# Optimization experiments

Measured on AMD Instinct MI355X. Metric: run time of the kernel, lower is better.

Reference implementation:

```python
import jax, jax.numpy as jnp
import numpy as np
import math

B, S, H, K = 512, 200, 256, 16

def setup_inputs() -> dict:
    key = jax.random.key(0)
    ks = jax.random.split(key, 8)
    scale = 1.0 / math.sqrt(H)
    return {
        "input_tensor": jax.random.normal(ks[0], (B, S, H), dtype=jnp.float32),
        "item_mask": jax.random.randint(ks[1], (B, S, 1), 0, 2) > 0,
        "time_f_w_matrix": jax.random.uniform(ks[2], (B, S, 1), dtype=jnp.float32),
        "W1": jax.random.normal(ks[3], (H, H), dtype=jnp.float32) * scale,
        "b1": jnp.zeros((H,), dtype=jnp.float32),
        "W2": jax.random.normal(ks[4], (H, H), dtype=jnp.float32) * scale,
        "b2": jnp.zeros((H,), dtype=jnp.float32),
        "W3": jax.random.normal(ks[5], (H, K), dtype=jnp.float32) * scale,
    }

def reference(input_tensor, item_mask, time_f_w_matrix, W1, b1, W2, b2, W3):
    # small MLP: two Linear+ReLU then bias-free Linear to k_interests
    h = jax.nn.relu(jnp.einsum('bsh,hd->bsd', input_tensor, W1) + b1)
    h = jax.nn.relu(jnp.einsum('bsh,hd->bsd', h, W2) + b2)
    D = jnp.einsum('bsh,hk->bsk', h, W3)              # [B,S,K]
    D = jax.nn.softmax(D, axis=-1)                    # softmax over interests
    mask = item_mask[:, :, 0:1]                       # [B,S,1] bool, broadcast over K
    D = jnp.where(mask, D, jnp.float32(-10000.0))
    D = D / jnp.float32(math.sqrt(K))
    D = jax.nn.softmax(D, axis=-2)                    # softmax over sequence
    D = time_f_w_matrix[:, :, 0:1] * D                # time weighting
    # einsum 'nij,nik->nkj': pool items into K interest vectors
    return jnp.einsum('bsh,bsk->bkh', input_tensor, D)
```

## Files before the change

### kernel.cpp

```cpp
#include <hip/hip_runtime.h>
#include <math.h>

#define HDIM 256
#define KDIM 16
#define SDIM 200
#define BDIM 512
#define NROWS (BDIM * SDIM)
#define TM 64

typedef __bf16 bf16x8 __attribute__((ext_vector_type(8)));
typedef __bf16 bf16x4 __attribute__((ext_vector_type(4)));
typedef float  f32x4  __attribute__((ext_vector_type(4)));

__global__ __launch_bounds__(256) void pack_all(
    const float* __restrict__ W1, const float* __restrict__ W2,
    const float* __restrict__ W3,
    __bf16* __restrict__ w1h, __bf16* __restrict__ w1l,
    __bf16* __restrict__ w2h, __bf16* __restrict__ w2l,
    __bf16* __restrict__ w3h, __bf16* __restrict__ w3l)
{
    int gid = blockIdx.x * 256 + threadIdx.x;
    const float* src;
    __bf16 *oh, *ol;
    int e, N;
    if (gid < 65536)       { src = W1; oh = w1h; ol = w1l; e = gid;          N = 256; }
    else if (gid < 131072) { src = W2; oh = w2h; ol = w2l; e = gid - 65536;  N = 256; }
    else if (gid < 135168) { src = W3; oh = w3h; ol = w3l; e = gid - 131072; N = 16;  }
    else return;

    int j  = e & 7;
    int n  = (e >> 3) & (N - 1);
    int kg = e >> 3; kg = (N == 256) ? (kg >> 8) : (kg >> 4);
    int k  = kg * 8 + j;
    float v = src[k * N + n];
    __bf16 h = (__bf16)v;
    oh[e] = h;
    ol[e] = (__bf16)(v - (float)h);
}

__global__ __launch_bounds__(256) void mlp_softk_mfma(
    const float* __restrict__ X, const int* __restrict__ mask,
    const __bf16* __restrict__ W1h, const __bf16* __restrict__ W1l,
    const float* __restrict__ b1,
    const __bf16* __restrict__ W2h, const __bf16* __restrict__ W2l,
    const float* __restrict__ b2,
    const __bf16* __restrict__ W3h, const __bf16* __restrict__ W3l,
    float* __restrict__ P)
{
    __shared__ __bf16 Ahi[TM * HDIM];
    __shared__ __bf16 Alo[TM * HDIM];

    const int tid  = threadIdx.x;
    const int lane = tid & 63;
    const int w    = tid >> 6;
    const int l15  = lane & 15;
    const int quad = lane >> 4;
    const long r0  = (long)blockIdx.x * TM;

    {
        const float4* Xt = (const float4*)(X + r0 * HDIM);
        #pragma unroll
        for (int t = 0; t < (TM * HDIM / 4) / 256; ++t) {
            int v4  = tid + t * 256;
            float4 f = Xt[v4];
            int row = v4 >> 6;
            int col = (v4 & 63) << 2;
            int kgs = (col >> 3) ^ (row & 31);
            int base = row * HDIM + kgs * 8 + (col & 7);
            __bf16 h0 = (__bf16)f.x, h1 = (__bf16)f.y,
                   h2 = (__bf16)f.z, h3 = (__bf16)f.w;
            bf16x4 hv = {h0, h1, h2, h3};
            bf16x4 lv = {(__bf16)(f.x - (float)h0), (__bf16)(f.y - (float)h1),
                         (__bf16)(f.z - (float)h2), (__bf16)(f.w - (float)h3)};
            *(bf16x4*)(&Ahi[base]) = hv;
            *(bf16x4*)(&Alo[base]) = lv;
        }
    }
    __syncthreads();

    f32x4 acc[4][4];

    auto layer = [&](const __bf16* __restrict__ Wh, const __bf16* __restrict__ Wl,
                     const float* __restrict__ bias) {
        #pragma unroll
        for (int mt = 0; mt < 4; ++mt)
            #pragma unroll
            for (int nt = 0; nt < 4; ++nt)
                acc[mt][nt] = (f32x4){0.f, 0.f, 0.f, 0.f};

        #pragma unroll
        for (int kc = 0; kc < 8; ++kc) {
            bf16x8 bh[4], bl[4];
            #pragma unroll
            for (int nt = 0; nt < 4; ++nt) {
                int n  = w * 64 + nt * 16 + l15;
                int kg = kc * 4 + quad;
                bh[nt] = *(const bf16x8*)(Wh + (kg * HDIM + n) * 8);
                bl[nt] = *(const bf16x8*)(Wl + (kg * HDIM + n) * 8);
            }
            #pragma unroll
            for (int mt = 0; mt < 4; ++mt) {
                int row = mt * 16 + l15;
                int kgs = (kc * 4 + quad) ^ (row & 31);
                bf16x8 ah = *(const bf16x8*)(&Ahi[row * HDIM + kgs * 8]);
                bf16x8 al = *(const bf16x8*)(&Alo[row * HDIM + kgs * 8]);
                #pragma unroll
                for (int nt = 0; nt < 4; ++nt) {
                    acc[mt][nt] = __builtin_amdgcn_mfma_f32_16x16x32_bf16(
                        bh[nt], ah, acc[mt][nt], 0, 0, 0);
                    acc[mt][nt] = __builtin_amdgcn_mfma_f32_16x16x32_bf16(
                        bh[nt], al, acc[mt][nt], 0, 0, 0);
                    acc[mt][nt] = __builtin_amdgcn_mfma_f32_16x16x32_bf16(
                        bl[nt], ah, acc[mt][nt], 0, 0, 0);
                }
            }
        }
        __syncthreads();

        f32x4 bias4[4];
        #pragma unroll
        for (int nt = 0; nt < 4; ++nt)
            bias4[nt] = *(const f32x4*)(bias + w * 64 + nt * 16 + quad * 4);

        #pragma unroll
        for (int mt = 0; mt < 4; ++mt)
            #pragma unroll
            for (int nt = 0; nt < 4; ++nt) {
                int m   = mt * 16 + l15;
                int g   = w * 8 + nt * 2 + (quad >> 1);
                int idx = m * HDIM + (((g ^ (m & 31)) * 8) + (quad & 1) * 4);
                bf16x4 hv, lv;
                #pragma unroll
                for (int r = 0; r < 4; ++r) {
                    float v = fmaxf(acc[mt][nt][r] + bias4[nt][r], 0.f);
                    __bf16 h = (__bf16)v;
                    hv[r] = h;
                    lv[r] = (__bf16)(v - (float)h);
                }
                *(bf16x4*)(&Ahi[idx]) = hv;
                *(bf16x4*)(&Alo[idx]) = lv;
            }
        __syncthreads();
    };

    layer(W1h, W1l, b1);
    layer(W2h, W2l, b2);

    {
        f32x4 lg = {0.f, 0.f, 0.f, 0.f};
        #pragma unroll
        for (int kc = 0; kc < 8; ++kc) {
            int row = w * 16 + l15;
            int kg  = kc * 4 + quad;
            int kgs = kg ^ (row & 31);
            bf16x8 ah = *(const bf16x8*)(&Ahi[row * HDIM + kgs * 8]);
            bf16x8 al = *(const bf16x8*)(&Alo[row * HDIM + kgs * 8]);
            bf16x8 bh = *(const bf16x8*)(W3h + (kg * KDIM + l15) * 8);
            bf16x8 bl = *(const bf16x8*)(W3l + (kg * KDIM + l15) * 8);
            lg = __builtin_amdgcn_mfma_f32_16x16x32_bf16(ah, bh, lg, 0, 0, 0);
            lg = __builtin_amdgcn_mfma_f32_16x16x32_bf16(al, bh, lg, 0, 0, 0);
            lg = __builtin_amdgcn_mfma_f32_16x16x32_bf16(ah, bl, lg, 0, 0, 0);
        }

        #pragma unroll
        for (int r = 0; r < 4; ++r) {
            float v  = lg[r];
            float mx = v;
            mx = fmaxf(mx, __shfl_xor(mx, 1));
            mx = fmaxf(mx, __shfl_xor(mx, 2));
            mx = fmaxf(mx, __shfl_xor(mx, 4));
            mx = fmaxf(mx, __shfl_xor(mx, 8));
            float e = __expf(v - mx);
            float s = e;
            s += __shfl_xor(s, 1);
            s += __shfl_xor(s, 2);
            s += __shfl_xor(s, 4);
            s += __shfl_xor(s, 8);
            int grow = (int)r0 + w * 16 + quad * 4 + r;
            int mv   = mask[grow];
            float ov = mv ? (e / s) * 0.25f : -2500.0f;
            P[(long)grow * KDIM + l15] = ov;
        }
    }
}

__global__ __launch_bounds__(512) void softs_agg_kernel(
    const float* __restrict__ X, const float* __restrict__ tf,
    const float* __restrict__ P, float* __restrict__ out)
{
    __shared__ float wl[SDIM * KDIM];
    __shared__ float tfl[SDIM];
    __shared__ float invk[KDIM];
    __shared__ float red[6 * 8 * HDIM];
    float* psum = red;

    const int tid = threadIdx.x;
    const int b   = blockIdx.x;

    const float* Pb = P + (long)b * SDIM * KDIM;
    float ps = 0.f;
    #pragma unroll
    for (int t = 0; t < 7; ++t) {
        int i = tid + t * 512;
        if (i < SDIM * KDIM) {
            float e = __expf(Pb[i]);
            wl[i] = e;
            ps += e;
        }
    }
    psum[tid] = ps;
    if (tid < SDIM) tfl[tid] = tf[b * SDIM + tid];
    __syncthreads();

    if (tid < KDIM) {
        float s = 0.f;
        #pragma unroll
        for (int g = 0; g < 32; ++g) s += psum[tid + g * 16];
        invk[tid] = 1.f / s;
    }
    __syncthreads();

    #pragma unroll
    for (int t = 0; t < 7; ++t) {
        int i = tid + t * 512;
        if (i < SDIM * KDIM) wl[i] *= tfl[i >> 4] * invk[i & 15];
    }
    __syncthreads();

    const int wv = tid >> 6;
    const int sq = wv >> 1;
    const int kh = wv & 1;
    const int ln = tid & 63;

    f32x4 acc[8];
    #pragma unroll
    for (int j = 0; j < 8; ++j) acc[j] = (f32x4){0.f, 0.f, 0.f, 0.f};

    const f32x4* Xb4 = (const f32x4*)(X + (long)b * SDIM * HDIM);
    const f32x4* wl4 = (const f32x4*)wl;
    const int s0 = sq * 50;
    #pragma unroll 5
    for (int si = 0; si < 50; ++si) {
        int s = s0 + si;
        f32x4 x  = Xb4[s * 64 + ln];
        f32x4 d0 = wl4[s * 4 + 2 * kh + 0];
        f32x4 d1 = wl4[s * 4 + 2 * kh + 1];
        #pragma unroll
        for (int j = 0; j < 4; ++j) {
            acc[j]     += x * d0[j];
            acc[4 + j] += x * d1[j];
        }
    }

    if (sq > 0) {
        float* rp = red + (((sq - 1) * 2 + kh) * 8) * HDIM;
        #pragma unroll
        for (int j = 0; j < 8; ++j)
            *(f32x4*)(rp + j * HDIM + 4 * ln) = acc[j];
    }
    __syncthreads();
    if (sq == 0) {
        #pragma unroll
        for (int p = 0; p < 3; ++p) {
            const float* rp = red + ((p * 2 + kh) * 8) * HDIM;
            #pragma unroll
            for (int j = 0; j < 8; ++j)
                acc[j] += *(const f32x4*)(rp + j * HDIM + 4 * ln);
        }
        float* ob = out + (long)b * KDIM * HDIM + kh * 8 * HDIM;
        #pragma unroll
        for (int j = 0; j < 8; ++j)
            *(f32x4*)(ob + j * HDIM + 4 * ln) = acc[j];
    }
}

extern "C" void kernel_launch(void* const* d_in, const int* in_sizes, int n_in,
                              void* d_out, int out_size, void* d_ws, size_t ws_size,
                              hipStream_t stream) {
    (void)in_sizes; (void)n_in; (void)out_size; (void)ws_size;
    const float* X    = (const float*)d_in[0];
    const int*   mask = (const int*)  d_in[1];
    const float* tf   = (const float*)d_in[2];
    const float* W1   = (const float*)d_in[3];
    const float* b1   = (const float*)d_in[4];
    const float* W2   = (const float*)d_in[5];
    const float* b2   = (const float*)d_in[6];
    const float* W3   = (const float*)d_in[7];
    float* out = (float*)d_out;

    char* ws = (char*)d_ws;
    float*  P   = (float*)ws;
    __bf16* w1h = (__bf16*)(ws + 6553600);
    __bf16* w1l = w1h + 65536;
    __bf16* w2h = w1l + 65536;
    __bf16* w2l = w2h + 65536;
    __bf16* w3h = w2l + 65536;
    __bf16* w3l = w3h + 4096;

    pack_all<<<528, 256, 0, stream>>>(W1, W2, W3, w1h, w1l, w2h, w2l, w3h, w3l);
    mlp_softk_mfma<<<NROWS / TM, 256, 0, stream>>>(X, mask, w1h, w1l, b1,
                                                   w2h, w2l, b2, w3h, w3l, P);
    softs_agg_kernel<<<BDIM, 512, 0, stream>>>(X, tf, P, out);
}
```

Baseline: 269.5 us.

## Fuse MLP, masked softmaxes and pooling into one per-batch kernel

Replaces the two-kernel pipeline with one kernel per batch element that runs the MLP over 32-row chunks, keeps the interest logits in shared memory, then does the sequence softmax and weighted pooling. This removes the global write and read of the intermediate probability tensor and one kernel launch. In exchange the grid shrinks to one block per batch, each chunk gives less weight reuse, and the pooling stage has fewer waves per batch, which reduces parallelism and latency hiding.

```diff
diff --git a/kernel.cpp b/kernel.cpp
--- a/kernel.cpp
+++ b/kernel.cpp
@@ -6,7 +6,7 @@
 #define SDIM 200
 #define BDIM 512
 #define NROWS (BDIM * SDIM)
-#define TM 64
+#define SPAD 208
 
 typedef __bf16 bf16x8 __attribute__((ext_vector_type(8)));
 typedef __bf16 bf16x4 __attribute__((ext_vector_type(4)));
@@ -38,239 +38,265 @@
     ol[e] = (__bf16)(v - (float)h);
 }
 
-__global__ __launch_bounds__(256) void mlp_softk_mfma(
+template<int ROWS>
+__device__ __forceinline__ void stage_x(
+    const float* __restrict__ X, long r0, int tid,
+    __bf16* __restrict__ Ahi, __bf16* __restrict__ Alo)
+{
+    const f32x4* Xg = (const f32x4*)X;
+    #pragma unroll
+    for (int t = 0; t < (ROWS * HDIM / 4) / 256; ++t) {
+        int v4  = tid + t * 256;
+        int row = v4 >> 6;
+        long grow = r0 + row;
+        if (grow > (long)NROWS - 1) grow = (long)NROWS - 1;
+        f32x4 f = Xg[grow * 64 + (v4 & 63)];
+        int col = (v4 & 63) << 2;
+        int kgs = (col >> 3) ^ (row & 31);
+        int base = row * HDIM + kgs * 8 + (col & 7);
+        __bf16 h0 = (__bf16)f[0], h1 = (__bf16)f[1],
+               h2 = (__bf16)f[2], h3 = (__bf16)f[3];
+        bf16x4 hv = {h0, h1, h2, h3};
+        bf16x4 lv = {(__bf16)(f[0] - (float)h0), (__bf16)(f[1] - (float)h1),
+                     (__bf16)(f[2] - (float)h2), (__bf16)(f[3] - (float)h3)};
+        *(bf16x4*)(&Ahi[base]) = hv;
+        *(bf16x4*)(&Alo[base]) = lv;
+    }
+}
+
+template<int MT>
+__device__ __forceinline__ void layer_t(
+    const __bf16* __restrict__ Wh, const __bf16* __restrict__ Wl,
+    const float* __restrict__ bias,
+    __bf16* __restrict__ Ahi, __bf16* __restrict__ Alo,
+    int w, int l15, int quad)
+{
+    f32x4 acc[MT][4];
+    #pragma unroll
+    for (int mt = 0; mt < MT; ++mt)
+        #pragma unroll
+        for (int nt = 0; nt < 4; ++nt)
+            acc[mt][nt] = (f32x4){0.f, 0.f, 0.f, 0.f};
+
+    #pragma unroll
+    for (int kc = 0; kc < 8; ++kc) {
+        bf16x8 bh[4], bl[4];
+        #pragma unroll
+        for (int nt = 0; nt < 4; ++nt) {
+            int n  = w * 64 + nt * 16 + l15;
+            int kg = kc * 4 + quad;
+            bh[nt] = *(const bf16x8*)(Wh + (kg * HDIM + n) * 8);
+            bl[nt] = *(const bf16x8*)(Wl + (kg * HDIM + n) * 8);
+        }
+        #pragma unroll
+        for (int mt = 0; mt < MT; ++mt) {
+            int row = mt * 16 + l15;
+            int kgs = (kc * 4 + quad) ^ (row & 31);
+            bf16x8 ah = *(const bf16x8*)(&Ahi[row * HDIM + kgs * 8]);
+            bf16x8 al = *(const bf16x8*)(&Alo[row * HDIM + kgs * 8]);
+            #pragma unroll
+            for (int nt = 0; nt < 4; ++nt) {
+                acc[mt][nt] = __builtin_amdgcn_mfma_f32_16x16x32_bf16(
+                    bh[nt], ah, acc[mt][nt], 0, 0, 0);
+                acc[mt][nt] = __builtin_amdgcn_mfma_f32_16x16x32_bf16(
+                    bh[nt], al, acc[mt][nt], 0, 0, 0);
+                acc[mt][nt] = __builtin_amdgcn_mfma_f32_16x16x32_bf16(
+                    bl[nt], ah, acc[mt][nt], 0, 0, 0);
+            }
+        }
+    }
+    __syncthreads();
+
+    f32x4 bias4[4];
+    #pragma unroll
+    for (int nt = 0; nt < 4; ++nt)
+        bias4[nt] = *(const f32x4*)(bias + w * 64 + nt * 16 + quad * 4);
+
+    #pragma unroll
+    for (int mt = 0; mt < MT; ++mt)
+        #pragma unroll
+        for (int nt = 0; nt < 4; ++nt) {
+            int m   = mt * 16 + l15;
+            int g   = w * 8 + nt * 2 + (quad >> 1);
+            int idx = m * HDIM + (((g ^ (m & 31)) * 8) + (quad & 1) * 4);
+            bf16x4 hv, lv;
+            #pragma unroll
+            for (int r = 0; r < 4; ++r) {
+                float v = fmaxf(acc[mt][nt][r] + bias4[nt][r], 0.f);
+                __bf16 h = (__bf16)v;
+                hv[r] = h;
+                lv[r] = (__bf16)(v - (float)h);
+            }
+            *(bf16x4*)(&Ahi[idx]) = hv;
+            *(bf16x4*)(&Alo[idx]) = lv;
+        }
+    __syncthreads();
+}
+
+__global__ __launch_bounds__(256) void fused_kernel(
     const float* __restrict__ X, const int* __restrict__ mask,
+    const float* __restrict__ tf,
     const __bf16* __restrict__ W1h, const __bf16* __restrict__ W1l,
     const float* __restrict__ b1,
     const __bf16* __restrict__ W2h, const __bf16* __restrict__ W2l,
     const float* __restrict__ b2,
     const __bf16* __restrict__ W3h, const __bf16* __restrict__ W3l,
-    float* __restrict__ P)
+    float* __restrict__ out)
 {
-    __shared__ __bf16 Ahi[TM * HDIM];
-    __shared__ __bf16 Alo[TM * HDIM];
+    __shared__ __bf16 Ahi[32 * HDIM];
+    __shared__ __bf16 Alo[32 * HDIM];
+    __shared__ float  Dl[SPAD * KDIM];
+    __shared__ float  part[256];
+    __shared__ float  tfl[SDIM];
+    __shared__ float  invk[KDIM];
 
     const int tid  = threadIdx.x;
     const int lane = tid & 63;
     const int w    = tid >> 6;
     const int l15  = lane & 15;
     const int quad = lane >> 4;
-    const long r0  = (long)blockIdx.x * TM;
-
-    {
-        const float4* Xt = (const float4*)(X + r0 * HDIM);
-        #pragma unroll
-        for (int t = 0; t < (TM * HDIM / 4) / 256; ++t) {
-            int v4  = tid + t * 256;
-            float4 f = Xt[v4];
-            int row = v4 >> 6;
-            int col = (v4 & 63) << 2;
-            int kgs = (col >> 3) ^ (row & 31);
-            int base = row * HDIM + kgs * 8 + (col & 7);
-            __bf16 h0 = (__bf16)f.x, h1 = (__bf16)f.y,
-                   h2 = (__bf16)f.z, h3 = (__bf16)f.w;
-            bf16x4 hv = {h0, h1, h2, h3};
-            bf16x4 lv = {(__bf16)(f.x - (float)h0), (__bf16)(f.y - (float)h1),
-                         (__bf16)(f.z - (float)h2), (__bf16)(f.w - (float)h3)};
-            *(bf16x4*)(&Ahi[base]) = hv;
-            *(bf16x4*)(&Alo[base]) = lv;
-        }
-    }
-    __syncthreads();
-
-    f32x4 acc[4][4];
-
-    auto layer = [&](const __bf16* __restrict__ Wh, const __bf16* __restrict__ Wl,
-                     const float* __restrict__ bias) {
-        #pragma unroll
-        for (int mt = 0; mt < 4; ++mt)
-            #pragma unroll
-            for (int nt = 0; nt < 4; ++nt)
-                acc[mt][nt] = (f32x4){0.f, 0.f, 0.f, 0.f};
-
-        #pragma unroll
-        for (int kc = 0; kc < 8; ++kc) {
-            bf16x8 bh[4], bl[4];
-            #pragma unroll
-            for (int nt = 0; nt < 4; ++nt) {
-                int n  = w * 64 + nt * 16 + l15;
-                int kg = kc * 4 + quad;
-                bh[nt] = *(const bf16x8*)(Wh + (kg * HDIM + n) * 8);
-                bl[nt] = *(const bf16x8*)(Wl + (kg * HDIM + n) * 8);
-            }
-            #pragma unroll
-            for (int mt = 0; mt < 4; ++mt) {
-                int row = mt * 16 + l15;
-                int kgs = (kc * 4 + quad) ^ (row & 31);
+    const int b    = blockIdx.x;
+    const long rb  = (long)b * SDIM;
+
+    #pragma unroll 1
+    for (int c = 0; c < 6; ++c) {
+        stage_x<32>(X, rb + c * 32, tid, Ahi, Alo);
+        __syncthreads();
+        layer_t<2>(W1h, W1l, b1, Ahi, Alo, w, l15, quad);
+        layer_t<2>(W2h, W2l, b2, Ahi, Alo, w, l15, quad);
+
+        if (w < 2) {
+            f32x4 lg = {0.f, 0.f, 0.f, 0.f};
+            #pragma unroll
+            for (int kc = 0; kc < 8; ++kc) {
+                int row = w * 16 + l15;
+                int kg  = kc * 4 + quad;
+                int kgs = kg ^ (row & 31);
                 bf16x8 ah = *(const bf16x8*)(&Ahi[row * HDIM + kgs * 8]);
                 bf16x8 al = *(const bf16x8*)(&Alo[row * HDIM + kgs * 8]);
-                #pragma unroll
-                for (int nt = 0; nt < 4; ++nt) {
-                    acc[mt][nt] = __builtin_amdgcn_mfma_f32_16x16x32_bf16(
-                        bh[nt], ah, acc[mt][nt], 0, 0, 0);
-                    acc[mt][nt] = __builtin_amdgcn_mfma_f32_16x16x32_bf16(
-                        bh[nt], al, acc[mt][nt], 0, 0, 0);
-                    acc[mt][nt] = __builtin_amdgcn_mfma_f32_16x16x32_bf16(
-                        bl[nt], ah, acc[mt][nt], 0, 0, 0);
-                }
-            }
-        }
-        __syncthreads();
-
-        f32x4 bias4[4];
-        #pragma unroll
-        for (int nt = 0; nt < 4; ++nt)
-            bias4[nt] = *(const f32x4*)(bias + w * 64 + nt * 16 + quad * 4);
-
-        #pragma unroll
-        for (int mt = 0; mt < 4; ++mt)
-            #pragma unroll
-            for (int nt = 0; nt < 4; ++nt) {
-                int m   = mt * 16 + l15;
-                int g   = w * 8 + nt * 2 + (quad >> 1);
-                int idx = m * HDIM + (((g ^ (m & 31)) * 8) + (quad & 1) * 4);
-                bf16x4 hv, lv;
-                #pragma unroll
-                for (int r = 0; r < 4; ++r) {
-                    float v = fmaxf(acc[mt][nt][r] + bias4[nt][r], 0.f);
-                    __bf16 h = (__bf16)v;
-                    hv[r] = h;
-                    lv[r] = (__bf16)(v - (float)h);
-                }
-                *(bf16x4*)(&Ahi[idx]) = hv;
-                *(bf16x4*)(&Alo[idx]) = lv;
-            }
-        __syncthreads();
-    };
-
-    layer(W1h, W1l, b1);
-    layer(W2h, W2l, b2);
+                bf16x8 bh = *(const bf16x8*)(W3h + (kg * KDIM + l15) * 8);
+                bf16x8 bl = *(const bf16x8*)(W3l + (kg * KDIM + l15) * 8);
+                lg = __builtin_amdgcn_mfma_f32_16x16x32_bf16(ah, bh, lg, 0, 0, 0);
+                lg = __builtin_amdgcn_mfma_f32_16x16x32_bf16(al, bh, lg, 0, 0, 0);
+                lg = __builtin_amdgcn_mfma_f32_16x16x32_bf16(ah, bl, lg, 0, 0, 0);
+            }
+            #pragma unroll
+            for (int r = 0; r < 4; ++r) {
+                float v  = lg[r];
+                float mx = v;
+                mx = fmaxf(mx, __shfl_xor(mx, 1));
+                mx = fmaxf(mx, __shfl_xor(mx, 2));
+                mx = fmaxf(mx, __shfl_xor(mx, 4));
+                mx = fmaxf(mx, __shfl_xor(mx, 8));
+                float e = __expf(v - mx);
+                float s = e;
+                s += __shfl_xor(s, 1);
+                s += __shfl_xor(s, 2);
+                s += __shfl_xor(s, 4);
+                s += __shfl_xor(s, 8);
+                int local = c * 32 + w * 16 + quad * 4 + r;
+                int mv = mask[rb + local];
+                Dl[local * KDIM + l15] = mv ? (e / s) * 0.25f : -2500.0f;
+            }
+        }
+        __syncthreads();
+    }
 
     {
-        f32x4 lg = {0.f, 0.f, 0.f, 0.f};
-        #pragma unroll
-        for (int kc = 0; kc < 8; ++kc) {
-            int row = w * 16 + l15;
-            int kg  = kc * 4 + quad;
-            int kgs = kg ^ (row & 31);
-            bf16x8 ah = *(const bf16x8*)(&Ahi[row * HDIM + kgs * 8]);
-            bf16x8 al = *(const bf16x8*)(&Alo[row * HDIM + kgs * 8]);
-            bf16x8 bh = *(const bf16x8*)(W3h + (kg * KDIM + l15) * 8);
-            bf16x8 bl = *(const bf16x8*)(W3l + (kg * KDIM + l15) * 8);
-            lg = __builtin_amdgcn_mfma_f32_16x16x32_bf16(ah, bh, lg, 0, 0, 0);
-            lg = __builtin_amdgcn_mfma_f32_16x16x32_bf16(al, bh, lg, 0, 0, 0);
-            lg = __builtin_amdgcn_mfma_f32_16x16x32_bf16(ah, bl, lg, 0, 0, 0);
-        }
-
-        #pragma unroll
-        for (int r = 0; r < 4; ++r) {
-            float v  = lg[r];
-            float mx = v;
-            mx = fmaxf(mx, __shfl_xor(mx, 1));
-            mx = fmaxf(mx, __shfl_xor(mx, 2));
-            mx = fmaxf(mx, __shfl_xor(mx, 4));
-            mx = fmaxf(mx, __shfl_xor(mx, 8));
-            float e = __expf(v - mx);
-            float s = e;
-            s += __shfl_xor(s, 1);
-            s += __shfl_xor(s, 2);
-            s += __shfl_xor(s, 4);
-            s += __shfl_xor(s, 8);
-            int grow = (int)r0 + w * 16 + quad * 4 + r;
-            int mv   = mask[grow];
-            float ov = mv ? (e / s) * 0.25f : -2500.0f;
-            P[(long)grow * KDIM + l15] = ov;
-        }
-    }
-}
-
-__global__ __launch_bounds__(512) void softs_agg_kernel(
-    const float* __restrict__ X, const float* __restrict__ tf,
-    const float* __restrict__ P, float* __restrict__ out)
-{
-    __shared__ float wl[SDIM * KDIM];
-    __shared__ float tfl[SDIM];
-    __shared__ float invk[KDIM];
-    __shared__ float red[6 * 8 * HDIM];
-    float* psum = red;
-
-    const int tid = threadIdx.x;
-    const int b   = blockIdx.x;
-
-    const float* Pb = P + (long)b * SDIM * KDIM;
-    float ps = 0.f;
-    #pragma unroll
-    for (int t = 0; t < 7; ++t) {
-        int i = tid + t * 512;
-        if (i < SDIM * KDIM) {
-            float e = __expf(Pb[i]);
-            wl[i] = e;
+        stage_x<16>(X, rb + 192, tid, Ahi, Alo);
+        __syncthreads();
+        layer_t<1>(W1h, W1l, b1, Ahi, Alo, w, l15, quad);
+        layer_t<1>(W2h, W2l, b2, Ahi, Alo, w, l15, quad);
+
+        if (w == 0) {
+            f32x4 lg = {0.f, 0.f, 0.f, 0.f};
+            #pragma unroll
+            for (int kc = 0; kc < 8; ++kc) {
+                int row = l15;
+                int kg  = kc * 4 + quad;
+                int kgs = kg ^ (row & 31);
+                bf16x8 ah = *(const bf16x8*)(&Ahi[row * HDIM + kgs * 8]);
+                bf16x8 al = *(const bf16x8*)(&Alo[row * HDIM + kgs * 8]);
+                bf16x8 bh = *(const bf16x8*)(W3h + (kg * KDIM + l15) * 8);
+                bf16x8 bl = *(const bf16x8*)(W3l + (kg * KDIM + l15) * 8);
+                lg = __builtin_amdgcn_mfma_f32_16x16x32_bf16(ah, bh, lg, 0, 0, 0);
+                lg = __builtin_amdgcn_mfma_f32_16x16x32_bf16(al, bh, lg, 0, 0, 0);
+                lg = __builtin_amdgcn_mfma_f32_16x16x32_bf16(ah, bl, lg, 0, 0, 0);
+            }
+            #pragma unroll
+            for (int r = 0; r < 4; ++r) {
+                float v  = lg[r];
+                float mx = v;
+                mx = fmaxf(mx, __shfl_xor(mx, 1));
+                mx = fmaxf(mx, __shfl_xor(mx, 2));
+                mx = fmaxf(mx, __shfl_xor(mx, 4));
+                mx = fmaxf(mx, __shfl_xor(mx, 8));
+                float e = __expf(v - mx);
+                float s = e;
+                s += __shfl_xor(s, 1);
+                s += __shfl_xor(s, 2);
+                s += __shfl_xor(s, 4);
+                s += __shfl_xor(s, 8);
+                int local = 192 + quad * 4 + r;
+                int mv = (local < SDIM) ? mask[rb + local] : 0;
+                Dl[local * KDIM + l15] = mv ? (e / s) * 0.25f : -2500.0f;
+            }
+        }
+        __syncthreads();
+    }
+
+    {
+        const int k = tid & 15, rg = tid >> 4;
+        float ps = 0.f;
+        #pragma unroll
+        for (int i = 0; i < SPAD / 16; ++i) {
+            int s = rg + i * 16;
+            float e = __expf(Dl[s * KDIM + k]);
+            Dl[s * KDIM + k] = e;
             ps += e;
         }
-    }
-    psum[tid] = ps;
-    if (tid < SDIM) tfl[tid] = tf[b * SDIM + tid];
-    __syncthreads();
-
-    if (tid < KDIM) {
-        float s = 0.f;
-        #pragma unroll
-        for (int g = 0; g < 32; ++g) s += psum[tid + g * 16];
-        invk[tid] = 1.f / s;
-    }
-    __syncthreads();
-
-    #pragma unroll
-    for (int t = 0; t < 7; ++t) {
-        int i = tid + t * 512;
-        if (i < SDIM * KDIM) wl[i] *= tfl[i >> 4] * invk[i & 15];
-    }
-    __syncthreads();
-
-    const int wv = tid >> 6;
-    const int sq = wv >> 1;
-    const int kh = wv & 1;
-    const int ln = tid & 63;
-
-    f32x4 acc[8];
-    #pragma unroll
-    for (int j = 0; j < 8; ++j) acc[j] = (f32x4){0.f, 0.f, 0.f, 0.f};
-
-    const f32x4* Xb4 = (const f32x4*)(X + (long)b * SDIM * HDIM);
-    const f32x4* wl4 = (const f32x4*)wl;
-    const int s0 = sq * 50;
-    #pragma unroll 5
-    for (int si = 0; si < 50; ++si) {
-        int s = s0 + si;
-        f32x4 x  = Xb4[s * 64 + ln];
-        f32x4 d0 = wl4[s * 4 + 2 * kh + 0];
-        f32x4 d1 = wl4[s * 4 + 2 * kh + 1];
-        #pragma unroll
-        for (int j = 0; j < 4; ++j) {
-            acc[j]     += x * d0[j];
-            acc[4 + j] += x * d1[j];
-        }
-    }
-
-    if (sq > 0) {
-        float* rp = red + (((sq - 1) * 2 + kh) * 8) * HDIM;
-        #pragma unroll
-        for (int j = 0; j < 8; ++j)
-            *(f32x4*)(rp + j * HDIM + 4 * ln) = acc[j];
-    }
-    __syncthreads();
-    if (sq == 0) {
-        #pragma unroll
-        for (int p = 0; p < 3; ++p) {
-            const float* rp = red + ((p * 2 + kh) * 8) * HDIM;
-            #pragma unroll
-            for (int j = 0; j < 8; ++j)
-                acc[j] += *(const f32x4*)(rp + j * HDIM + 4 * ln);
-        }
-        float* ob = out + (long)b * KDIM * HDIM + kh * 8 * HDIM;
-        #pragma unroll
-        for (int j = 0; j < 8; ++j)
-            *(f32x4*)(ob + j * HDIM + 4 * ln) = acc[j];
+        part[tid] = ps;
+        if (tid < SDIM) tfl[tid] = tf[rb + tid];
+        __syncthreads();
+
+        if (tid < KDIM) {
+            float s = 0.f;
+            #pragma unroll
+            for (int g = 0; g < 16; ++g) s += part[tid + g * 16];
+            invk[tid] = 1.f / s;
+        }
+        __syncthreads();
+
+        #pragma unroll
+        for (int i = 0; i < SPAD / 16; ++i) {
+            int s = rg + i * 16;
+            float t = (s < SDIM) ? tfl[s] : 0.f;
+            Dl[s * KDIM + k] *= t * invk[k];
+        }
+        __syncthreads();
+    }
+
+    {
+        f32x4 a4[4];
+        #pragma unroll
+        for (int j = 0; j < 4; ++j) a4[j] = (f32x4){0.f, 0.f, 0.f, 0.f};
+
+        const f32x4* Xb4 = (const f32x4*)(X + rb * HDIM);
+        const int soff = w * 50;
+        #pragma unroll 5
+        for (int si = 0; si < SDIM; ++si) {
+            int s = si + soff;
+            if (s >= SDIM) s -= SDIM;
+            f32x4 x = Xb4[s * 64 + lane];
+            f32x4 d = *(const f32x4*)(&Dl[s * KDIM + w * 4]);
+            #pragma unroll
+            for (int j = 0; j < 4; ++j) a4[j] += x * d[j];
+        }
+
+        float* ob = out + ((long)b * KDIM + w * 4) * HDIM;
+        #pragma unroll
+        for (int j = 0; j < 4; ++j)
+            *(f32x4*)(ob + j * HDIM + 4 * lane) = a4[j];
     }
 }
 
@@ -289,8 +315,7 @@
     float* out = (float*)d_out;
 
     char* ws = (char*)d_ws;
-    float*  P   = (float*)ws;
-    __bf16* w1h = (__bf16*)(ws + 6553600);
+    __bf16* w1h = (__bf16*)ws;
     __bf16* w1l = w1h + 65536;
     __bf16* w2h = w1l + 65536;
     __bf16* w2l = w2h + 65536;
@@ -298,7 +323,6 @@
     __bf16* w3l = w3h + 4096;
 
     pack_all<<<528, 256, 0, stream>>>(W1, W2, W3, w1h, w1l, w2h, w2l, w3h, w3l);
-    mlp_softk_mfma<<<NROWS / TM, 256, 0, stream>>>(X, mask, w1h, w1l, b1,
-                                                   w2h, w2l, b2, w3h, w3l, P);
-    softs_agg_kernel<<<BDIM, 512, 0, stream>>>(X, tf, P, out);
-}
+    fused_kernel<<<BDIM, 256, 0, stream>>>(X, mask, tf, w1h, w1l, b1,
+                                           w2h, w2l, b2, w3h, w3l, out);
+}
```

After: 643.5 us. 139% more time.
